# Performance work log

Measured on AMD Instinct MI355X. Metric: run time of the kernel, lower is better.

The kernel has to match this reference:

```python
import jax, jax.numpy as jnp
import numpy as np

L = 6        # gnn_layers
H = 4        # heads
C = 128      # per-head channels = hidden // heads
HID = 512    # hidden
IN = 768     # in_dim
N = 20000    # nodes
E = 320000   # edges
P = 100000   # scored pairs


def _gelu(v):
    return jax.nn.gelu(v, approximate=False)


def _ln(v, g, b):
    m = v.mean(-1, keepdims=True)
    var = v.var(-1, keepdims=True)
    return (v - m) / jnp.sqrt(var + 1e-5) * g + b


def setup_inputs() -> dict:
    key = jax.random.key(0)
    ks = jax.random.split(key, 24)
    g = lambda k, shape, s=0.02: (jax.random.normal(k, shape, jnp.float32) * s)
    inp = {}
    inp["x"] = jax.random.normal(ks[0], (N, IN), jnp.float32)
    inp["edge_index"] = jax.random.randint(ks[1], (2, E), 0, N)
    inp["edges"] = jax.random.randint(ks[2], (2, P), 0, N)
    # FeatureMixer (no alt branch)
    inp["mixer_W"] = g(ks[3], (IN, HID)); inp["mixer_b"] = jnp.zeros((HID,), jnp.float32)
    # Stacked TransformerConv params per layer
    inp["Wq"] = g(ks[4], (L, HID, HID)); inp["bq"] = jnp.zeros((L, HID), jnp.float32)
    inp["Wk"] = g(ks[5], (L, HID, HID)); inp["bk"] = jnp.zeros((L, HID), jnp.float32)
    inp["Wv"] = g(ks[6], (L, HID, HID)); inp["bv"] = jnp.zeros((L, HID), jnp.float32)
    inp["Ws"] = g(ks[7], (L, HID, HID)); inp["bs"] = jnp.zeros((L, HID), jnp.float32)  # lin_skip (root weight)
    inp["ln_g"] = jnp.ones((L, HID), jnp.float32); inp["ln_b"] = jnp.zeros((L, HID), jnp.float32)
    # Dual projections
    inp["syn_W"] = g(ks[8], (HID, HID)); inp["syn_b"] = jnp.zeros((HID,), jnp.float32)
    inp["ant_W"] = g(ks[9], (HID, HID)); inp["ant_b"] = jnp.zeros((HID,), jnp.float32)
    # Bilinear score matrices
    inp["W_syn"] = g(ks[10], (HID, HID), 0.04)
    inp["W_ant"] = g(ks[11], (HID, HID), 0.04)
    # Gate MLP: Linear(4*HID, HID) -> GELU -> Linear(HID, 1) -> Sigmoid
    inp["gW1"] = g(ks[12], (4 * HID, HID)); inp["gb1"] = jnp.zeros((HID,), jnp.float32)
    inp["gW2"] = g(ks[13], (HID, 1)); inp["gb2"] = jnp.zeros((1,), jnp.float32)
    return inp


def reference(x, edge_index, edges, mixer_W, mixer_b, Wq, bq, Wk, bk, Wv, bv,
              Ws, bs, ln_g, ln_b, syn_W, syn_b, ant_W, ant_b, W_syn, W_ant,
              gW1, gb1, gW2, gb2):
    src, dst = edge_index[0], edge_index[1]
    scale = 1.0 / np.sqrt(C).astype(np.float32)
    # FeatureMixer (eval mode: dropout = identity)
    h = _gelu(x @ mixer_W + mixer_b)  # [N, HID]
    for l in range(L):
        # node-side projections, then gather per edge
        q = (h @ Wq[l] + bq[l]).reshape(N, H, C)
        k = (h @ Wk[l] + bk[l]).reshape(N, H, C)
        v = (h @ Wv[l] + bv[l]).reshape(N, H, C)
        logits = (q[dst] * k[src]).sum(-1) * scale          # [E, H]
        mx = jax.ops.segment_max(logits, dst, num_segments=N)   # [N, H]
        ex = jnp.exp(logits - mx[dst])
        den = jax.ops.segment_sum(ex, dst, num_segments=N)      # [N, H]
        alpha = ex / den[dst]                                   # segment softmax over incoming edges
        msg = alpha[..., None] * v[src]                         # [E, H, C]
        out = jax.ops.segment_sum(msg, dst, num_segments=N).reshape(N, HID)
        out = out + h @ Ws[l] + bs[l]                           # root/skip term of TransformerConv
        out = _gelu(out)
        h = _ln(h + out, ln_g[l], ln_b[l])
    z_syn = _gelu(h @ syn_W + syn_b)
    z_ant = _gelu(h @ ant_W + ant_b)
    i, j = edges[0], edges[1]
    vi_s, vj_s = z_syn[i], z_syn[j]
    vi_a, vj_a = z_ant[i], z_ant[j]
    s_syn = ((vi_s @ W_syn) * vj_s).sum(-1)
    s_ant = ((vi_a @ W_ant) * vj_a).sum(-1)
    pair = jnp.concatenate([jnp.abs(vi_s - vj_s), vi_s * vj_s,
                            jnp.abs(vi_a - vj_a), vi_a * vj_a], axis=-1)  # [P, 4*HID]
    g = jax.nn.sigmoid(_gelu(pair @ gW1 + gb1) @ gW2 + gb2).squeeze(-1)
    return g * s_ant + (1.0 - g) * (-s_syn)
```

## Files before the change

### kernel.cpp

```cpp
#include <hip/hip_runtime.h>
#include <cstdint>

#define L_LAYERS 6

typedef __attribute__((ext_vector_type(8))) short bf16x8;
typedef __attribute__((ext_vector_type(4))) float f32x4;
typedef __attribute__((ext_vector_type(2))) float f32x2;

__device__ __forceinline__ float gelu1(float v) {
    return 0.5f * v * (1.0f + erff(v * 0.7071067811865475f));
}

__device__ __forceinline__ unsigned int f2bf2(float a, float b) {
    union { float f; unsigned u; } x, y;
    x.f = a; y.f = b;
    unsigned lo = (x.u + 0x7FFFu + ((x.u >> 16) & 1u)) >> 16;
    unsigned hi = (y.u + 0x7FFFu + ((y.u >> 16) & 1u)) & 0xFFFF0000u;
    return lo | hi;
}

__device__ __forceinline__ unsigned short f2bf1(float a) {
    union { float f; unsigned u; } x;
    x.f = a;
    return (unsigned short)((x.u + 0x7FFFu + ((x.u >> 16) & 1u)) >> 16);
}

__device__ __forceinline__ float2 bfp2(unsigned u) {
    union { unsigned u; float f; } a, b;
    a.u = u << 16;
    b.u = u & 0xFFFF0000u;
    return make_float2(a.f, b.f);
}

__device__ __forceinline__ void gload16(const void* g, void* l) {
    __builtin_amdgcn_global_load_lds(
        (const __attribute__((address_space(1))) void*)g,
        (__attribute__((address_space(3))) void*)l, 16, 0, 0);
}


__global__ void k_zero(int* __restrict__ p, int n) {
    int i = blockIdx.x * 256 + threadIdx.x;
    if (i < n) p[i] = 0;
}


__global__ void k_hist(const int* __restrict__ dst, int* __restrict__ hist, int E) {
    int e = blockIdx.x * 256 + threadIdx.x;
    if (e < E) atomicAdd(&hist[dst[e]], 1);
}

__global__ __launch_bounds__(1024) void k_scan(const int* __restrict__ hist,
                                               int* __restrict__ off, int n) {
    __shared__ int buf[1024];
    __shared__ int carry;
    int tid = threadIdx.x;
    if (tid == 0) carry = 0;
    __syncthreads();
    for (int base = 0; base < n; base += 1024) {
        int v = (base + tid < n) ? hist[base + tid] : 0;
        buf[tid] = v;
        __syncthreads();
        int x = v;
        for (int o = 1; o < 1024; o <<= 1) {
            int t = (tid >= o) ? buf[tid - o] : 0;
            __syncthreads();
            x += t;
            buf[tid] = x;
            __syncthreads();
        }
        int c = carry;
        if (base + tid < n) off[base + tid] = c + x - v;
        __syncthreads();
        if (tid == 1023) carry = c + buf[1023];
        __syncthreads();
    }
    if (tid == 0) off[n] = carry;
}

__global__ void k_scatter(const int* __restrict__ src, const int* __restrict__ dst,
                          const int* __restrict__ off, int* __restrict__ cursor,
                          int* __restrict__ srcS, int E) {
    int e = blockIdx.x * 256 + threadIdx.x;
    if (e < E) {
        int d = dst[e];
        int pos = off[d] + atomicAdd(&cursor[d], 1);
        srcS[pos] = src[e];
    }
}


__global__ void k_wcat(const float* __restrict__ Wq, const float* __restrict__ Wk,
                       const float* __restrict__ Wv, const float* __restrict__ Ws,
                       short* __restrict__ Wt) {
    int idx = blockIdx.x * 256 + threadIdx.x;
    int k = idx & 511;
    int nf = (idx >> 9) & 2047;
    int l = idx >> 20;
    int sel = nf >> 9, nn = nf & 511;
    const float* W = (sel == 0) ? Wq : (sel == 1) ? Wk : (sel == 2) ? Wv : Ws;
    float v = W[((size_t)l * 512 + k) * 512 + nn];
    Wt[idx] = (short)f2bf1(v);
}

__global__ void k_tr(const float* __restrict__ W, short* __restrict__ Wt, int K, int N,
                     int swz) {
    int k = blockIdx.x * 256 + threadIdx.x;
    int n = blockIdx.y;
    if (k < K) {
        int kk = k;
        if (swz) kk = (k & ~31) | (((((k >> 3) & 3) ^ ((n >> 1) & 3))) << 3) | (k & 7);
        Wt[(size_t)n * K + kk] = (short)f2bf1(W[(size_t)k * N + n]);
    }
}

__global__ void k_bcat(const float* __restrict__ bq, const float* __restrict__ bk,
                       const float* __restrict__ bv, const float* __restrict__ bs,
                       float* __restrict__ bcat) {
    int idx = blockIdx.x * 256 + threadIdx.x;
    if (idx >= L_LAYERS * 2048) return;
    int l = idx >> 11, n = idx & 2047;
    int sel = n >> 9, nn = n & 511;
    const float* b = (sel == 0) ? bq : (sel == 1) ? bk : (sel == 2) ? bv : bs;
    bcat[idx] = b[l * 512 + nn];
}

__global__ void k_bdual(const float* __restrict__ sb, const float* __restrict__ ab,
                        float* __restrict__ bd) {
    int idx = blockIdx.x * 256 + threadIdx.x;
    if (idx < 1024) bd[idx] = (idx < 512) ? sb[idx] : ab[idx - 512];
}


__global__ __launch_bounds__(256) void gemm_a32(
    const float* __restrict__ A, int lda,
    const short* __restrict__ Bt,
    const float* __restrict__ bias,
    float* __restrict__ Cf, short* __restrict__ Cbf, int ldc,
    int M, int N, int K, int act) {
    __shared__ __align__(16) short As[128][40];
    __shared__ __align__(16) short Bs[128][40];
    const int tid = threadIdx.x;
    const int lane = tid & 63;
    const int wave = tid >> 6;
    const int wr = (wave >> 1) * 64;
    const int wc = (wave & 1) * 64;
    const int l16 = lane & 15;
    const int quad = lane >> 4;
    const int row0 = blockIdx.x * 128;
    const int col0 = blockIdx.y * 128;
    const int sr = tid >> 2;
    const int sk = (tid & 3) * 8;

    f32x4 acc[4][4];
#pragma unroll
    for (int i = 0; i < 4; ++i)
#pragma unroll
        for (int j = 0; j < 4; ++j)
            acc[i][j] = f32x4{0.f, 0.f, 0.f, 0.f};

    for (int kb = 0; kb < K; kb += 32) {
#pragma unroll
        for (int hh = 0; hh < 2; ++hh) {
            int r = sr + hh * 64;
            int gr = row0 + r;
            float4 a0, a1;
            if (gr < M) {
                const float* p = A + (size_t)gr * lda + kb + sk;
                a0 = *(const float4*)p;
                a1 = *(const float4*)(p + 4);
            } else {
                a0 = make_float4(0.f, 0.f, 0.f, 0.f);
                a1 = make_float4(0.f, 0.f, 0.f, 0.f);
            }
            uint4 av;
            av.x = f2bf2(a0.x, a0.y);
            av.y = f2bf2(a0.z, a0.w);
            av.z = f2bf2(a1.x, a1.y);
            av.w = f2bf2(a1.z, a1.w);
            *(uint4*)&As[r][sk] = av;
            const short* bp = Bt + (size_t)(col0 + r) * K + kb + sk;
            *(uint4*)&Bs[r][sk] = *(const uint4*)bp;
        }
        __syncthreads();
        bf16x8 af[4], bfr[4];
#pragma unroll
        for (int i = 0; i < 4; ++i)
            af[i] = *(const bf16x8*)&As[wr + i * 16 + l16][quad * 8];
#pragma unroll
        for (int j = 0; j < 4; ++j)
            bfr[j] = *(const bf16x8*)&Bs[wc + j * 16 + l16][quad * 8];
#pragma unroll
        for (int i = 0; i < 4; ++i)
#pragma unroll
            for (int j = 0; j < 4; ++j)
                acc[i][j] = __builtin_amdgcn_mfma_f32_16x16x32_bf16(af[i], bfr[j], acc[i][j], 0, 0, 0);
        __syncthreads();
    }
#pragma unroll
    for (int i = 0; i < 4; ++i) {
        int rbase = row0 + wr + i * 16 + quad * 4;
#pragma unroll
        for (int j = 0; j < 4; ++j) {
            int c = col0 + wc + j * 16 + l16;
            float bv = bias ? bias[c] : 0.0f;
#pragma unroll
            for (int rg = 0; rg < 4; ++rg) {
                int gr = rbase + rg;
                if (gr < M) {
                    float v = acc[i][j][rg] + bv;
                    if (act) v = gelu1(v);
                    Cf[(size_t)gr * ldc + c] = v;
                    if (Cbf) Cbf[(size_t)gr * ldc + c] = (short)f2bf1(v);
                }
            }
        }
    }
}


__global__ __launch_bounds__(256) void gemm_bb(
    const short* __restrict__ A, int lda,
    const short* __restrict__ Bt,
    const float* __restrict__ bias,
    short* __restrict__ C, unsigned char* __restrict__ C8, int ldc,
    int M, int N, int K, int act) {
    __shared__ __align__(16) short As[128 * 32];
    __shared__ __align__(16) short Bs[128 * 32];
    const int tid = threadIdx.x;
    const int lane = tid & 63;
    const int wave = tid >> 6;
    const int wr = (wave >> 1) * 64;
    const int wc = (wave & 1) * 64;
    const int l16 = lane & 15;
    const int quad = lane >> 4;
    const int row0 = blockIdx.x * 128;
    const int col0 = blockIdx.y * 128;
    const int c0 = tid, c1 = tid + 256;
    const int r0 = c0 >> 2, kq0 = (c0 & 3) * 8;
    const int r1 = c1 >> 2, kq1 = (c1 & 3) * 8;
    int ga0 = row0 + r0; if (ga0 >= M) ga0 = M - 1;
    int ga1 = row0 + r1; if (ga1 >= M) ga1 = M - 1;
    const short* Ap0 = A + (size_t)ga0 * lda + kq0;
    const short* Ap1 = A + (size_t)ga1 * lda + kq1;
    const short* Bp0 = Bt + (size_t)(col0 + r0) * K + kq0;
    const short* Bp1 = Bt + (size_t)(col0 + r1) * K + kq1;

    f32x4 acc[4][4];
#pragma unroll
    for (int i = 0; i < 4; ++i)
#pragma unroll
        for (int j = 0; j < 4; ++j)
            acc[i][j] = f32x4{0.f, 0.f, 0.f, 0.f};

    for (int kb = 0; kb < K; kb += 32) {
        gload16(Ap0 + kb, &As[c0 * 8]);
        gload16(Ap1 + kb, &As[c1 * 8]);
        gload16(Bp0 + kb, &Bs[c0 * 8]);
        gload16(Bp1 + kb, &Bs[c1 * 8]);
        __syncthreads();
        bf16x8 af[4], bfr[4];
#pragma unroll
        for (int i = 0; i < 4; ++i)
            af[i] = *(const bf16x8*)&As[(wr + i * 16 + l16) * 32 + quad * 8];
#pragma unroll
        for (int j = 0; j < 4; ++j)
            bfr[j] = *(const bf16x8*)&Bs[(wc + j * 16 + l16) * 32 + quad * 8];
#pragma unroll
        for (int i = 0; i < 4; ++i)
#pragma unroll
            for (int j = 0; j < 4; ++j)
                acc[i][j] = __builtin_amdgcn_mfma_f32_16x16x32_bf16(af[i], bfr[j], acc[i][j], 0, 0, 0);
        __syncthreads();
    }
#pragma unroll
    for (int i = 0; i < 4; ++i) {
        int rbase = row0 + wr + i * 16 + quad * 4;
#pragma unroll
        for (int j = 0; j < 4; ++j) {
            int c = col0 + wc + j * 16 + l16;
            float bv = bias ? bias[c] : 0.0f;
#pragma unroll
            for (int rg = 0; rg < 4; ++rg) {
                int gr = rbase + rg;
                if (gr < M) {
                    float v = acc[i][j][rg] + bv;
                    if (act) v = gelu1(v);
                    C[(size_t)gr * ldc + c] = (short)f2bf1(v);
                    if (C8) {
                        int r8 = __builtin_amdgcn_cvt_pk_fp8_f32(v, v, 0, false);
                        C8[(size_t)gr * ldc + c] = (unsigned char)(r8 & 0xFF);
                    }
                }
            }
        }
    }
}


__global__ __launch_bounds__(256) void gemm_qkvs(
    const short* __restrict__ A,
    const short* __restrict__ Bt,
    const float* __restrict__ bias,
    short* __restrict__ qvs,
    unsigned char* __restrict__ kv8,
    int M, int mtiles) {
    const int K = 512;
    const int id = blockIdx.x;
    const int xcd = id & 7;
    const int t = id >> 3;
    const int col_t = t & 15;
    const int row_t = (t >> 4) * 8 + xcd;
    if (row_t >= mtiles) return;
    const int row0 = row_t * 128;
    const int col0 = col_t * 128;
    __shared__ __align__(16) short As[128 * 32];
    __shared__ __align__(16) short Bs[128 * 32];
    const int tid = threadIdx.x;
    const int lane = tid & 63;
    const int wave = tid >> 6;
    const int wr = (wave >> 1) * 64;
    const int wc = (wave & 1) * 64;
    const int l16 = lane & 15;
    const int quad = lane >> 4;
    const int c0 = tid, c1 = tid + 256;
    const int r0 = c0 >> 2, kq0 = (c0 & 3) * 8;
    const int r1 = c1 >> 2, kq1 = (c1 & 3) * 8;
    int ga0 = row0 + r0; if (ga0 >= M) ga0 = M - 1;
    int ga1 = row0 + r1; if (ga1 >= M) ga1 = M - 1;
    const short* Ap0 = A + (size_t)ga0 * K + kq0;
    const short* Ap1 = A + (size_t)ga1 * K + kq1;
    const short* Bp0 = Bt + (size_t)(col0 + r0) * K + kq0;
    const short* Bp1 = Bt + (size_t)(col0 + r1) * K + kq1;

    f32x4 acc[4][4];
#pragma unroll
    for (int i = 0; i < 4; ++i)
#pragma unroll
        for (int j = 0; j < 4; ++j)
            acc[i][j] = f32x4{0.f, 0.f, 0.f, 0.f};

    for (int kb = 0; kb < K; kb += 32) {
        gload16(Ap0 + kb, &As[c0 * 8]);
        gload16(Ap1 + kb, &As[c1 * 8]);
        gload16(Bp0 + kb, &Bs[c0 * 8]);
        gload16(Bp1 + kb, &Bs[c1 * 8]);
        __syncthreads();
        bf16x8 af[4], bfr[4];
#pragma unroll
        for (int i = 0; i < 4; ++i)
            af[i] = *(const bf16x8*)&As[(wr + i * 16 + l16) * 32 + quad * 8];
#pragma unroll
        for (int j = 0; j < 4; ++j)
            bfr[j] = *(const bf16x8*)&Bs[(wc + j * 16 + l16) * 32 + quad * 8];
#pragma unroll
        for (int i = 0; i < 4; ++i)
#pragma unroll
            for (int j = 0; j < 4; ++j)
                acc[i][j] = __builtin_amdgcn_mfma_f32_16x16x32_bf16(af[i], bfr[j], acc[i][j], 0, 0, 0);
        __syncthreads();
    }
#pragma unroll
    for (int i = 0; i < 4; ++i) {
        int rbase = row0 + wr + i * 16 + quad * 4;
#pragma unroll
        for (int j = 0; j < 4; ++j) {
            int c = col0 + wc + j * 16 + l16;
            int sec = c >> 9;
            int cc = c & 511;
            float bv = bias[c];
#pragma unroll
            for (int rg = 0; rg < 4; ++rg) {
                int gr = rbase + rg;
                if (gr < M) {
                    float v = acc[i][j][rg] + bv;
                    if (sec == 1 || sec == 2) {
                        int r8 = __builtin_amdgcn_cvt_pk_fp8_f32(v, v, 0, false);
                        int off = (sec == 1) ? cc : 512 + cc;
                        kv8[(size_t)gr * 1024 + off] = (unsigned char)(r8 & 0xFF);
                    } else {
                        int off = (sec == 0) ? cc : 512 + cc;
                        qvs[(size_t)gr * 1024 + off] = (short)f2bf1(v);
                    }
                }
            }
        }
    }
}


__global__ __launch_bounds__(256, 3) void gemm_gate(
    const unsigned char* __restrict__ z8,
    const int* __restrict__ pi, const int* __restrict__ pj, int P,
    const short* __restrict__ Bt,
    const float* __restrict__ gb1,
    const float* __restrict__ gW2,
    float* __restrict__ gpart, int ptiles) {
    __shared__ __align__(16) short Aab[64 * 32];
    __shared__ __align__(16) short Amu[64 * 32];
    __shared__ __align__(16) short Bab[256 * 32];
    __shared__ __align__(16) short Bmu[256 * 32];
    __shared__ int iArr[64];
    __shared__ int jArr[64];
    __shared__ float rowsum[64];
    const int id = blockIdx.x;
    const int xcd = id & 7;
    const int t = id >> 3;
    const int col_t = t & 1;
    const int row_t = (t >> 1) * 8 + xcd;
    if (row_t >= ptiles) return;
    const int row0 = row_t * 64;
    const int col0 = col_t * 256;
    const int tid = threadIdx.x;
    const int lane = tid & 63;
    const int wave = tid >> 6;
    const int wc = wave * 64;
    const int l16 = lane & 15;
    const int quad = lane >> 4;
    const int sr = tid >> 2;
    const int sk = (tid & 3) * 8;
    const int qs = (quad ^ ((l16 >> 1) & 3)) * 8;
    const int awoff = sr * 32 + (((tid & 3) ^ ((sr >> 1) & 3)) << 3);

    if (tid < 64) {
        int p = row0 + tid;
        int ok = (p < P);
        iArr[tid] = ok ? pi[p] : 0;
        jArr[tid] = ok ? pj[p] : 0;
        rowsum[tid] = 0.0f;
    }
    __syncthreads();
    const unsigned char* zi = z8 + (size_t)iArr[sr] * 1024 + sk;
    const unsigned char* zj = z8 + (size_t)jArr[sr] * 1024 + sk;
    const short* bp0 = Bt + (size_t)(col0 + sr) * 2048 + sk;

    f32x4 acc[4][4];
#pragma unroll
    for (int i = 0; i < 4; ++i)
#pragma unroll
        for (int j = 0; j < 4; ++j)
            acc[i][j] = f32x4{0.f, 0.f, 0.f, 0.f};

    for (int part = 0; part < 2; ++part) {
        for (int c = 0; c < 512; c += 32) {
            const short* bp = bp0 + part * 1024 + c;
#pragma unroll
            for (int hh = 0; hh < 4; ++hh) {
                const short* q = bp + (size_t)hh * 64 * 2048;
                gload16(q, &Bab[hh * 2048 + tid * 8]);
                gload16(q + 512, &Bmu[hh * 2048 + tid * 8]);
            }
            uint2 xu = *(const uint2*)(zi + part * 512 + c);
            uint2 yu = *(const uint2*)(zj + part * 512 + c);
            f32x2 x0 = __builtin_amdgcn_cvt_pk_f32_fp8((int)xu.x, false);
            f32x2 x1 = __builtin_amdgcn_cvt_pk_f32_fp8((int)xu.x, true);
            f32x2 x2 = __builtin_amdgcn_cvt_pk_f32_fp8((int)xu.y, false);
            f32x2 x3 = __builtin_amdgcn_cvt_pk_f32_fp8((int)xu.y, true);
            f32x2 y0 = __builtin_amdgcn_cvt_pk_f32_fp8((int)yu.x, false);
            f32x2 y1 = __builtin_amdgcn_cvt_pk_f32_fp8((int)yu.x, true);
            f32x2 y2 = __builtin_amdgcn_cvt_pk_f32_fp8((int)yu.y, false);
            f32x2 y3 = __builtin_amdgcn_cvt_pk_f32_fp8((int)yu.y, true);
            uint4 aa, am;
            aa.x = f2bf2(fabsf(x0.x - y0.x), fabsf(x0.y - y0.y));
            aa.y = f2bf2(fabsf(x1.x - y1.x), fabsf(x1.y - y1.y));
            aa.z = f2bf2(fabsf(x2.x - y2.x), fabsf(x2.y - y2.y));
            aa.w = f2bf2(fabsf(x3.x - y3.x), fabsf(x3.y - y3.y));
            am.x = f2bf2(x0.x * y0.x, x0.y * y0.y);
            am.y = f2bf2(x1.x * y1.x, x1.y * y1.y);
            am.z = f2bf2(x2.x * y2.x, x2.y * y2.y);
            am.w = f2bf2(x3.x * y3.x, x3.y * y3.y);
            *(uint4*)&Aab[awoff] = aa;
            *(uint4*)&Amu[awoff] = am;
            __syncthreads();
            bf16x8 af[4];
#pragma unroll
            for (int i = 0; i < 4; ++i)
                af[i] = *(const bf16x8*)&Aab[(i * 16 + l16) * 32 + qs];
#pragma unroll
            for (int j = 0; j < 4; ++j) {
                bf16x8 bf = *(const bf16x8*)&Bab[(wc + j * 16 + l16) * 32 + qs];
#pragma unroll
                for (int i = 0; i < 4; ++i)
                    acc[i][j] = __builtin_amdgcn_mfma_f32_16x16x32_bf16(af[i], bf, acc[i][j], 0, 0, 0);
            }
#pragma unroll
            for (int i = 0; i < 4; ++i)
                af[i] = *(const bf16x8*)&Amu[(i * 16 + l16) * 32 + qs];
#pragma unroll
            for (int j = 0; j < 4; ++j) {
                bf16x8 bf = *(const bf16x8*)&Bmu[(wc + j * 16 + l16) * 32 + qs];
#pragma unroll
                for (int i = 0; i < 4; ++i)
                    acc[i][j] = __builtin_amdgcn_mfma_f32_16x16x32_bf16(af[i], bf, acc[i][j], 0, 0, 0);
            }
            __syncthreads();
        }
    }
#pragma unroll
    for (int i = 0; i < 4; ++i) {
#pragma unroll
        for (int rg = 0; rg < 4; ++rg) {
            float partial = 0.f;
#pragma unroll
            for (int j = 0; j < 4; ++j) {
                int cc = col0 + wc + j * 16 + l16;
                partial += gelu1(acc[i][j][rg] + gb1[cc]) * gW2[cc];
            }
            partial += __shfl_xor(partial, 1);
            partial += __shfl_xor(partial, 2);
            partial += __shfl_xor(partial, 4);
            partial += __shfl_xor(partial, 8);
            if (l16 == 0)
                atomicAdd(&rowsum[i * 16 + quad * 4 + rg], partial);
        }
    }
    __syncthreads();
    if (tid < 64 && (row0 + tid) < P)
        atomicAdd(&gpart[row0 + tid], rowsum[tid]);
}


__global__ __launch_bounds__(256) void k_attn(const short* __restrict__ qvs,
                                              const unsigned char* __restrict__ kv8,
                                              const int* __restrict__ srcS,
                                              const int* __restrict__ offs,
                                              float* __restrict__ h,
                                              short* __restrict__ h_bf,
                                              const float* __restrict__ lng,
                                              const float* __restrict__ lnb, int Nn) {
    const int tid = threadIdx.x;
    const int lane = tid & 63;
    const int wv = tid >> 6;
    const int n = blockIdx.x * 4 + wv;
    if (n >= Nn) return;
    const int st = offs[n], en = offs[n + 1];
    const size_t chOff = (size_t)lane * 8;

    uint4 qv = *(const uint4*)(qvs + (size_t)n * 1024 + chOff);
    float2 q0 = bfp2(qv.x), q1 = bfp2(qv.y), q2 = bfp2(qv.z), q3 = bfp2(qv.w);
    float acc[8];
#pragma unroll
    for (int i = 0; i < 8; ++i) acc[i] = 0.f;
    float m_l = -3.4e38f, l_l = 0.f;

    for (int e0 = st; e0 < en; e0 += 64) {
        int cnt = min(64, en - e0);
        int myS = (lane < cnt) ? srcS[e0 + lane] : 0;
        for (int ei = 0; ei < cnt; ++ei) {
            int s = __shfl(myS, ei);
            const unsigned char* srow = kv8 + (size_t)s * 1024 + chOff;
            uint2 kq = *(const uint2*)srow;
            uint2 vq = *(const uint2*)(srow + 512);
            f32x2 k0 = __builtin_amdgcn_cvt_pk_f32_fp8((int)kq.x, false);
            f32x2 k1 = __builtin_amdgcn_cvt_pk_f32_fp8((int)kq.x, true);
            f32x2 k2 = __builtin_amdgcn_cvt_pk_f32_fp8((int)kq.y, false);
            f32x2 k3 = __builtin_amdgcn_cvt_pk_f32_fp8((int)kq.y, true);
            float d = q0.x * k0.x + q0.y * k0.y + q1.x * k1.x + q1.y * k1.y +
                      q2.x * k2.x + q2.y * k2.y + q3.x * k3.x + q3.y * k3.y;
            d += __shfl_xor(d, 1);
            d += __shfl_xor(d, 2);
            d += __shfl_xor(d, 4);
            d += __shfl_xor(d, 8);
            float lg = d * 0.08838834764831845f;
            float m_new = fmaxf(m_l, lg);
            float sc = __expf(m_l - m_new);
            float p = __expf(lg - m_new);
            l_l = l_l * sc + p;
            m_l = m_new;
            f32x2 v0 = __builtin_amdgcn_cvt_pk_f32_fp8((int)vq.x, false);
            f32x2 v1 = __builtin_amdgcn_cvt_pk_f32_fp8((int)vq.x, true);
            f32x2 v2 = __builtin_amdgcn_cvt_pk_f32_fp8((int)vq.y, false);
            f32x2 v3 = __builtin_amdgcn_cvt_pk_f32_fp8((int)vq.y, true);
            acc[0] = acc[0] * sc + p * v0.x; acc[1] = acc[1] * sc + p * v0.y;
            acc[2] = acc[2] * sc + p * v1.x; acc[3] = acc[3] * sc + p * v1.y;
            acc[4] = acc[4] * sc + p * v2.x; acc[5] = acc[5] * sc + p * v2.y;
            acc[6] = acc[6] * sc + p * v3.x; acc[7] = acc[7] * sc + p * v3.y;
        }
    }
    float rinv = (en > st) ? 1.0f / l_l : 0.f;
    uint4 su = *(const uint4*)(qvs + (size_t)n * 1024 + 512 + chOff);
    float2 s0 = bfp2(su.x), s1 = bfp2(su.y), s2 = bfp2(su.z), s3 = bfp2(su.w);
    float sv[8] = {s0.x, s0.y, s1.x, s1.y, s2.x, s2.y, s3.x, s3.y};
    const float* hp = h + (size_t)n * 512 + chOff;
    float4 h0 = *(const float4*)hp;
    float4 h1 = *(const float4*)(hp + 4);
    float hv[8] = {h0.x, h0.y, h0.z, h0.w, h1.x, h1.y, h1.z, h1.w};
    float r[8];
    float sum = 0.f, ssq = 0.f;
#pragma unroll
    for (int i = 0; i < 8; ++i) {
        r[i] = hv[i] + gelu1(acc[i] * rinv + sv[i]);
        sum += r[i];
        ssq += r[i] * r[i];
    }
    for (int o = 32; o; o >>= 1) {
        sum += __shfl_xor(sum, o);
        ssq += __shfl_xor(ssq, o);
    }
    float mean = sum * (1.0f / 512.0f);
    float var = ssq * (1.0f / 512.0f) - mean * mean;
    float inv = rsqrtf(var + 1e-5f);
    const float* gp = lng + chOff;
    const float* bp = lnb + chOff;
    float4 g0 = *(const float4*)gp, g1 = *(const float4*)(gp + 4);
    float4 b0 = *(const float4*)bp, b1 = *(const float4*)(bp + 4);
    float ga[8] = {g0.x, g0.y, g0.z, g0.w, g1.x, g1.y, g1.z, g1.w};
    float ba[8] = {b0.x, b0.y, b0.z, b0.w, b1.x, b1.y, b1.z, b1.w};
    float o8[8];
#pragma unroll
    for (int i = 0; i < 8; ++i) o8[i] = (r[i] - mean) * inv * ga[i] + ba[i];
    float* hw = h + (size_t)n * 512 + chOff;
    *(float4*)hw = make_float4(o8[0], o8[1], o8[2], o8[3]);
    *(float4*)(hw + 4) = make_float4(o8[4], o8[5], o8[6], o8[7]);
    uint4 ob;
    ob.x = f2bf2(o8[0], o8[1]);
    ob.y = f2bf2(o8[2], o8[3]);
    ob.z = f2bf2(o8[4], o8[5]);
    ob.w = f2bf2(o8[6], o8[7]);
    *(uint4*)(h_bf + (size_t)n * 512 + chOff) = ob;
}


__global__ __launch_bounds__(256) void k_pairscore(const short* __restrict__ z,
                                                   const short* __restrict__ t,
                                                   const int* __restrict__ pi,
                                                   const int* __restrict__ pj,
                                                   float* __restrict__ ssyn,
                                                   float* __restrict__ sant, int P) {
    int p = blockIdx.x * 4 + (threadIdx.x >> 6);
    if (p >= P) return;
    int lane = threadIdx.x & 63;
    int i = pi[p], j = pj[p];
    uint4 a = *(const uint4*)(t + (size_t)i * 1024 + lane * 8);
    uint4 b = *(const uint4*)(z + (size_t)j * 1024 + lane * 8);
    float2 a0 = bfp2(a.x), a1 = bfp2(a.y), a2 = bfp2(a.z), a3 = bfp2(a.w);
    float2 b0 = bfp2(b.x), b1 = bfp2(b.y), b2 = bfp2(b.z), b3 = bfp2(b.w);
    float ds = a0.x * b0.x + a0.y * b0.y + a1.x * b1.x + a1.y * b1.y +
               a2.x * b2.x + a2.y * b2.y + a3.x * b3.x + a3.y * b3.y;
    uint4 c = *(const uint4*)(t + (size_t)i * 1024 + 512 + lane * 8);
    uint4 d = *(const uint4*)(z + (size_t)j * 1024 + 512 + lane * 8);
    float2 c0 = bfp2(c.x), c1 = bfp2(c.y), c2 = bfp2(c.z), c3 = bfp2(c.w);
    float2 d0 = bfp2(d.x), d1 = bfp2(d.y), d2 = bfp2(d.z), d3 = bfp2(d.w);
    float da = c0.x * d0.x + c0.y * d0.y + c1.x * d1.x + c1.y * d1.y +
               c2.x * d2.x + c2.y * d2.y + c3.x * d3.x + c3.y * d3.y;
    for (int o = 32; o; o >>= 1) {
        ds += __shfl_xor(ds, o);
        da += __shfl_xor(da, o);
    }
    if (lane == 0) { ssyn[p] = ds; sant[p] = da; }
}


__global__ void k_final(const float* __restrict__ gpart, const float* __restrict__ gb2,
                        const float* __restrict__ ssyn, const float* __restrict__ sant,
                        float* __restrict__ out, int P) {
    int p = blockIdx.x * 256 + threadIdx.x;
    if (p < P) {
        float s = 1.0f / (1.0f + __expf(-(gpart[p] + gb2[0])));
        out[p] = s * sant[p] - (1.0f - s) * ssyn[p];
    }
}


extern "C" void kernel_launch(void* const* d_in, const int* in_sizes, int n_in,
                              void* d_out, int out_size, void* d_ws, size_t ws_size,
                              hipStream_t stream) {
    const float* x = (const float*)d_in[0];
    const int* ei = (const int*)d_in[1];
    const int* pe = (const int*)d_in[2];
    const float* mixer_W = (const float*)d_in[3];
    const float* mixer_b = (const float*)d_in[4];
    const float* Wq = (const float*)d_in[5];
    const float* bq = (const float*)d_in[6];
    const float* Wk = (const float*)d_in[7];
    const float* bk = (const float*)d_in[8];
    const float* Wv = (const float*)d_in[9];
    const float* bv = (const float*)d_in[10];
    const float* Ws = (const float*)d_in[11];
    const float* bs = (const float*)d_in[12];
    const float* ln_g = (const float*)d_in[13];
    const float* ln_b = (const float*)d_in[14];
    const float* syn_W = (const float*)d_in[15];
    const float* syn_b = (const float*)d_in[16];
    const float* ant_W = (const float*)d_in[17];
    const float* ant_b = (const float*)d_in[18];
    const float* W_syn = (const float*)d_in[19];
    const float* W_ant = (const float*)d_in[20];
    const float* gW1 = (const float*)d_in[21];
    const float* gb1 = (const float*)d_in[22];
    const float* gW2 = (const float*)d_in[23];
    const float* gb2 = (const float*)d_in[24];
    float* out = (float*)d_out;

    const int Nn = in_sizes[0] / 768;
    const int E = in_sizes[1] / 2;
    const int P = in_sizes[2] / 2;

    char* w = (char*)d_ws;
    auto alloc = [&](size_t bytes) -> char* {
        char* p = w;
        w += (bytes + 255) & ~(size_t)255;
        return p;
    };
    float* h = (float*)alloc((size_t)Nn * 512 * 4);
    short* h_bf = (short*)alloc((size_t)Nn * 512 * 2);
    char* U = alloc((size_t)Nn * 2048 * 2);
    short* qvs = (short*)U;
    unsigned char* kv8 = (unsigned char*)(U + (size_t)Nn * 1024 * 2);
    short* zB = (short*)U;
    short* tB = (short*)(U + (size_t)Nn * 1024 * 2);
    unsigned char* z8 = (unsigned char*)alloc((size_t)Nn * 1024);
    float* ssyn = (float*)alloc((size_t)P * 3 * 4);
    float* sant = ssyn + P;
    float* gpart = ssyn + 2 * P;
    int* srcS = (int*)alloc((size_t)E * 4);
    int* hist = (int*)alloc((size_t)Nn * 2 * 4);
    int* cursor = hist + Nn;
    int* offs = (int*)alloc((size_t)(Nn + 1) * 4);
    short* mixWt = (short*)alloc((size_t)512 * 768 * 2);
    short* wcat = (short*)alloc((size_t)L_LAYERS * 2048 * 512 * 2);
    short* dualWt = (short*)alloc((size_t)1024 * 512 * 2);
    short* bilWt = (short*)alloc((size_t)1024 * 512 * 2);
    short* gw1t = (short*)alloc((size_t)512 * 2048 * 2);
    float* bcat = (float*)alloc((size_t)L_LAYERS * 2048 * 4);
    float* bdual = (float*)alloc((size_t)1024 * 4);

    k_zero<<<(2 * Nn + 255) / 256, 256, 0, stream>>>(hist, 2 * Nn);
    k_hist<<<(E + 255) / 256, 256, 0, stream>>>(ei + E, hist, E);
    k_scan<<<1, 1024, 0, stream>>>(hist, offs, Nn);
    k_scatter<<<(E + 255) / 256, 256, 0, stream>>>(ei, ei + E, offs, cursor, srcS, E);

    k_wcat<<<(L_LAYERS * 2048 * 512) / 256, 256, 0, stream>>>(Wq, Wk, Wv, Ws, wcat);
    k_tr<<<dim3(3, 512), 256, 0, stream>>>(mixer_W, mixWt, 768, 512, 0);
    k_tr<<<dim3(2, 512), 256, 0, stream>>>(syn_W, dualWt, 512, 512, 0);
    k_tr<<<dim3(2, 512), 256, 0, stream>>>(ant_W, dualWt + 512 * 512, 512, 512, 0);
    k_tr<<<dim3(2, 512), 256, 0, stream>>>(W_syn, bilWt, 512, 512, 0);
    k_tr<<<dim3(2, 512), 256, 0, stream>>>(W_ant, bilWt + 512 * 512, 512, 512, 0);
    k_tr<<<dim3(8, 512), 256, 0, stream>>>(gW1, gw1t, 2048, 512, 1);
    k_bcat<<<48, 256, 0, stream>>>(bq, bk, bv, bs, bcat);
    k_bdual<<<4, 256, 0, stream>>>(syn_b, ant_b, bdual);

    const int mtiles = (Nn + 127) / 128;
    gemm_a32<<<dim3(mtiles, 4), 256, 0, stream>>>(x, 768, mixWt, mixer_b, h, h_bf, 512,
                                                  Nn, 512, 768, 1);

    const int qk_grid = ((mtiles + 7) / 8) * 8 * 16;
    for (int l = 0; l < L_LAYERS; ++l) {
        gemm_qkvs<<<qk_grid, 256, 0, stream>>>(h_bf, wcat + (size_t)l * 2048 * 512,
                                               bcat + l * 2048, qvs, kv8, Nn, mtiles);
        k_attn<<<(Nn + 3) / 4, 256, 0, stream>>>(qvs, kv8, srcS, offs, h, h_bf,
                                                 ln_g + l * 512, ln_b + l * 512, Nn);
    }

    gemm_bb<<<dim3(mtiles, 8), 256, 0, stream>>>(h_bf, 512, dualWt, bdual, zB, z8, 1024,
                                                 Nn, 1024, 512, 1);
    gemm_bb<<<dim3(mtiles, 4), 256, 0, stream>>>(zB, 1024, bilWt, nullptr, tB, nullptr, 1024,
                                                 Nn, 512, 512, 0);
    gemm_bb<<<dim3(mtiles, 4), 256, 0, stream>>>(zB + 512, 1024, bilWt + 512 * 512, nullptr,
                                                 tB + 512, nullptr, 1024, Nn, 512, 512, 0);

    k_pairscore<<<(P + 3) / 4, 256, 0, stream>>>(zB, tB, pe, pe + P, ssyn, sant, P);

    k_zero<<<(P + 255) / 256, 256, 0, stream>>>((int*)gpart, P);
    const int ptiles = (P + 63) / 64;
    const int gate_grid = ((ptiles + 7) / 8) * 8 * 2;
    gemm_gate<<<gate_grid, 256, 0, stream>>>(z8, pe, pe + P, P,
                                             gw1t, gb1, gW2, gpart, ptiles);
    k_final<<<(P + 255) / 256, 256, 0, stream>>>(gpart, gb2, ssyn, sant, out, P);
}
```

Before: 1.681 ms.

## Retile gate GEMM to full-width 128x512 tiles and drop atomic partial sums

Restructures the gate MLP GEMM so each 512-thread block computes all 512 output columns for 128 pairs. This removes the two-column-tile split, the zeroing kernel and the global atomics, and gathers the pair features once per block instead of twice. It also prefetches the next fp8 feature chunk into registers and uses the hardware packed bf16 convert instead of manual rounding. In exchange it needs much larger accumulator state per thread (4x8 MFMA tiles) and a bigger LDS B buffer, which raises register pressure and can limit occupancy.

```diff
diff --git a/kernel.cpp b/kernel.cpp
--- a/kernel.cpp
+++ b/kernel.cpp
@@ -23,6 +23,12 @@
     union { float f; unsigned u; } x;
     x.f = a;
     return (unsigned short)((x.u + 0x7FFFu + ((x.u >> 16) & 1u)) >> 16);
+}
+
+__device__ __forceinline__ unsigned cvt_pk_bf16(float lo, float hi) {
+    unsigned r;
+    asm("v_cvt_pk_bf16_f32 %0, %1, %2" : "=v"(r) : "v"(lo), "v"(hi));
+    return r;
 }
 
 __device__ __forceinline__ float2 bfp2(unsigned u) {
@@ -389,40 +395,32 @@
 }
 
 
-__global__ __launch_bounds__(256, 3) void gemm_gate(
+__global__ __launch_bounds__(512, 6) void gemm_gate(
     const unsigned char* __restrict__ z8,
     const int* __restrict__ pi, const int* __restrict__ pj, int P,
     const short* __restrict__ Bt,
     const float* __restrict__ gb1,
     const float* __restrict__ gW2,
-    float* __restrict__ gpart, int ptiles) {
-    __shared__ __align__(16) short Aab[64 * 32];
-    __shared__ __align__(16) short Amu[64 * 32];
-    __shared__ __align__(16) short Bab[256 * 32];
-    __shared__ __align__(16) short Bmu[256 * 32];
-    __shared__ int iArr[64];
-    __shared__ int jArr[64];
-    __shared__ float rowsum[64];
-    const int id = blockIdx.x;
-    const int xcd = id & 7;
-    const int t = id >> 3;
-    const int col_t = t & 1;
-    const int row_t = (t >> 1) * 8 + xcd;
-    if (row_t >= ptiles) return;
-    const int row0 = row_t * 64;
-    const int col0 = col_t * 256;
+    float* __restrict__ gpart) {
+    __shared__ __align__(16) short Bs[512 * 32];
+    __shared__ __align__(16) short As[128 * 32];
+    __shared__ int iArr[128];
+    __shared__ int jArr[128];
+    __shared__ float rowsum[128];
+    const int row0 = blockIdx.x * 128;
     const int tid = threadIdx.x;
     const int lane = tid & 63;
     const int wave = tid >> 6;
-    const int wc = wave * 64;
+    const int wm = wave >> 2;
+    const int wn = wave & 3;
     const int l16 = lane & 15;
     const int quad = lane >> 4;
-    const int sr = tid >> 2;
-    const int sk = (tid & 3) * 8;
+    const int arow = tid >> 2;
+    const int aslot = tid & 3;
     const int qs = (quad ^ ((l16 >> 1) & 3)) * 8;
-    const int awoff = sr * 32 + (((tid & 3) ^ ((sr >> 1) & 3)) << 3);
-
-    if (tid < 64) {
+    const int awoff = arow * 32 + ((aslot ^ ((arow >> 1) & 3)) << 3);
+
+    if (tid < 128) {
         int p = row0 + tid;
         int ok = (p < P);
         iArr[tid] = ok ? pi[p] : 0;
@@ -430,71 +428,85 @@
         rowsum[tid] = 0.0f;
     }
     __syncthreads();
-    const unsigned char* zi = z8 + (size_t)iArr[sr] * 1024 + sk;
-    const unsigned char* zj = z8 + (size_t)jArr[sr] * 1024 + sk;
-    const short* bp0 = Bt + (size_t)(col0 + sr) * 2048 + sk;
-
-    f32x4 acc[4][4];
+    const unsigned char* zi = z8 + (size_t)iArr[arow] * 1024 + aslot * 8;
+    const unsigned char* zj = z8 + (size_t)jArr[arow] * 1024 + aslot * 8;
+    const short* brow = Bt + (size_t)(tid >> 2) * 2048 + (tid & 3) * 8;
+
+    f32x4 acc[4][8];
 #pragma unroll
     for (int i = 0; i < 4; ++i)
 #pragma unroll
-        for (int j = 0; j < 4; ++j)
+        for (int j = 0; j < 8; ++j)
             acc[i][j] = f32x4{0.f, 0.f, 0.f, 0.f};
 
-    for (int part = 0; part < 2; ++part) {
-        for (int c = 0; c < 512; c += 32) {
-            const short* bp = bp0 + part * 1024 + c;
-#pragma unroll
-            for (int hh = 0; hh < 4; ++hh) {
-                const short* q = bp + (size_t)hh * 64 * 2048;
-                gload16(q, &Bab[hh * 2048 + tid * 8]);
-                gload16(q + 512, &Bmu[hh * 2048 + tid * 8]);
-            }
-            uint2 xu = *(const uint2*)(zi + part * 512 + c);
-            uint2 yu = *(const uint2*)(zj + part * 512 + c);
-            f32x2 x0 = __builtin_amdgcn_cvt_pk_f32_fp8((int)xu.x, false);
-            f32x2 x1 = __builtin_amdgcn_cvt_pk_f32_fp8((int)xu.x, true);
-            f32x2 x2 = __builtin_amdgcn_cvt_pk_f32_fp8((int)xu.y, false);
-            f32x2 x3 = __builtin_amdgcn_cvt_pk_f32_fp8((int)xu.y, true);
-            f32x2 y0 = __builtin_amdgcn_cvt_pk_f32_fp8((int)yu.x, false);
-            f32x2 y1 = __builtin_amdgcn_cvt_pk_f32_fp8((int)yu.x, true);
-            f32x2 y2 = __builtin_amdgcn_cvt_pk_f32_fp8((int)yu.y, false);
-            f32x2 y3 = __builtin_amdgcn_cvt_pk_f32_fp8((int)yu.y, true);
-            uint4 aa, am;
-            aa.x = f2bf2(fabsf(x0.x - y0.x), fabsf(x0.y - y0.y));
-            aa.y = f2bf2(fabsf(x1.x - y1.x), fabsf(x1.y - y1.y));
-            aa.z = f2bf2(fabsf(x2.x - y2.x), fabsf(x2.y - y2.y));
-            aa.w = f2bf2(fabsf(x3.x - y3.x), fabsf(x3.y - y3.y));
-            am.x = f2bf2(x0.x * y0.x, x0.y * y0.y);
-            am.y = f2bf2(x1.x * y1.x, x1.y * y1.y);
-            am.z = f2bf2(x2.x * y2.x, x2.y * y2.y);
-            am.w = f2bf2(x3.x * y3.x, x3.y * y3.y);
-            *(uint4*)&Aab[awoff] = aa;
-            *(uint4*)&Amu[awoff] = am;
-            __syncthreads();
+    uint2 xu = *(const uint2*)zi;
+    uint2 yu = *(const uint2*)zj;
+
+    for (int kc = 0; kc < 32; ++kc) {
+        const int chb = ((kc >> 4) << 10) + ((kc & 15) << 5);
+#pragma unroll
+        for (int g = 0; g < 4; ++g)
+            gload16(brow + (size_t)(g * 128) * 2048 + chb, &Bs[(g * 512 + tid) * 8]);
+        uint2 xn, yn;
+        if (kc + 1 < 32) {
+            int koff = (((kc + 1) >> 4) << 9) + (((kc + 1) & 15) << 5);
+            xn = *(const uint2*)(zi + koff);
+            yn = *(const uint2*)(zj + koff);
+        }
+        f32x2 x0 = __builtin_amdgcn_cvt_pk_f32_fp8((int)xu.x, false);
+        f32x2 x1 = __builtin_amdgcn_cvt_pk_f32_fp8((int)xu.x, true);
+        f32x2 x2 = __builtin_amdgcn_cvt_pk_f32_fp8((int)xu.y, false);
+        f32x2 x3 = __builtin_amdgcn_cvt_pk_f32_fp8((int)xu.y, true);
+        f32x2 y0 = __builtin_amdgcn_cvt_pk_f32_fp8((int)yu.x, false);
+        f32x2 y1 = __builtin_amdgcn_cvt_pk_f32_fp8((int)yu.x, true);
+        f32x2 y2 = __builtin_amdgcn_cvt_pk_f32_fp8((int)yu.y, false);
+        f32x2 y3 = __builtin_amdgcn_cvt_pk_f32_fp8((int)yu.y, true);
+        uint4 aa, am;
+        aa.x = cvt_pk_bf16(fabsf(x0.x - y0.x), fabsf(x0.y - y0.y));
+        aa.y = cvt_pk_bf16(fabsf(x1.x - y1.x), fabsf(x1.y - y1.y));
+        aa.z = cvt_pk_bf16(fabsf(x2.x - y2.x), fabsf(x2.y - y2.y));
+        aa.w = cvt_pk_bf16(fabsf(x3.x - y3.x), fabsf(x3.y - y3.y));
+        am.x = cvt_pk_bf16(x0.x * y0.x, x0.y * y0.y);
+        am.y = cvt_pk_bf16(x1.x * y1.x, x1.y * y1.y);
+        am.z = cvt_pk_bf16(x2.x * y2.x, x2.y * y2.y);
+        am.w = cvt_pk_bf16(x3.x * y3.x, x3.y * y3.y);
+        *(uint4*)&As[awoff] = aa;
+        __syncthreads();
+        {
             bf16x8 af[4];
 #pragma unroll
             for (int i = 0; i < 4; ++i)
-                af[i] = *(const bf16x8*)&Aab[(i * 16 + l16) * 32 + qs];
-#pragma unroll
-            for (int j = 0; j < 4; ++j) {
-                bf16x8 bf = *(const bf16x8*)&Bab[(wc + j * 16 + l16) * 32 + qs];
+                af[i] = *(const bf16x8*)&As[(wm * 64 + i * 16 + l16) * 32 + qs];
+#pragma unroll
+            for (int j = 0; j < 8; ++j) {
+                bf16x8 bf = *(const bf16x8*)&Bs[(wn * 128 + j * 16 + l16) * 32 + qs];
 #pragma unroll
                 for (int i = 0; i < 4; ++i)
                     acc[i][j] = __builtin_amdgcn_mfma_f32_16x16x32_bf16(af[i], bf, acc[i][j], 0, 0, 0);
             }
+        }
+        __syncthreads();
+#pragma unroll
+        for (int g = 0; g < 4; ++g)
+            gload16(brow + (size_t)(g * 128) * 2048 + chb + 512, &Bs[(g * 512 + tid) * 8]);
+        *(uint4*)&As[awoff] = am;
+        __syncthreads();
+        {
+            bf16x8 af[4];
 #pragma unroll
             for (int i = 0; i < 4; ++i)
-                af[i] = *(const bf16x8*)&Amu[(i * 16 + l16) * 32 + qs];
-#pragma unroll
-            for (int j = 0; j < 4; ++j) {
-                bf16x8 bf = *(const bf16x8*)&Bmu[(wc + j * 16 + l16) * 32 + qs];
+                af[i] = *(const bf16x8*)&As[(wm * 64 + i * 16 + l16) * 32 + qs];
+#pragma unroll
+            for (int j = 0; j < 8; ++j) {
+                bf16x8 bf = *(const bf16x8*)&Bs[(wn * 128 + j * 16 + l16) * 32 + qs];
 #pragma unroll
                 for (int i = 0; i < 4; ++i)
                     acc[i][j] = __builtin_amdgcn_mfma_f32_16x16x32_bf16(af[i], bf, acc[i][j], 0, 0, 0);
             }
-            __syncthreads();
-        }
+        }
+        __syncthreads();
+        xu = xn;
+        yu = yn;
     }
 #pragma unroll
     for (int i = 0; i < 4; ++i) {
@@ -502,8 +514,8 @@
         for (int rg = 0; rg < 4; ++rg) {
             float partial = 0.f;
 #pragma unroll
-            for (int j = 0; j < 4; ++j) {
-                int cc = col0 + wc + j * 16 + l16;
+            for (int j = 0; j < 8; ++j) {
+                int cc = wn * 128 + j * 16 + l16;
                 partial += gelu1(acc[i][j][rg] + gb1[cc]) * gW2[cc];
             }
             partial += __shfl_xor(partial, 1);
@@ -511,12 +523,14 @@
             partial += __shfl_xor(partial, 4);
             partial += __shfl_xor(partial, 8);
             if (l16 == 0)
-                atomicAdd(&rowsum[i * 16 + quad * 4 + rg], partial);
+                atomicAdd(&rowsum[wm * 64 + i * 16 + quad * 4 + rg], partial);
         }
     }
     __syncthreads();
-    if (tid < 64 && (row0 + tid) < P)
-        atomicAdd(&gpart[row0 + tid], rowsum[tid]);
+    if (tid < 128) {
+        int p = row0 + tid;
+        if (p < P) gpart[p] = rowsum[tid];
+    }
 }
 
 
@@ -761,10 +775,7 @@
 
     k_pairscore<<<(P + 3) / 4, 256, 0, stream>>>(zB, tB, pe, pe + P, ssyn, sant, P);
 
-    k_zero<<<(P + 255) / 256, 256, 0, stream>>>((int*)gpart, P);
-    const int ptiles = (P + 63) / 64;
-    const int gate_grid = ((ptiles + 7) / 8) * 8 * 2;
-    gemm_gate<<<gate_grid, 256, 0, stream>>>(z8, pe, pe + P, P,
-                                             gw1t, gb1, gW2, gpart, ptiles);
+    const int ptiles2 = (P + 127) / 128;
+    gemm_gate<<<ptiles2, 512, 0, stream>>>(z8, pe, pe + P, P, gw1t, gb1, gW2, gpart);
     k_final<<<(P + 255) / 256, 256, 0, stream>>>(gpart, gb2, ssyn, sant, out, P);
 }
```

Result: slower. 4.824 ms (+186.9%).
